# Performance work log

Hardware: AMD Instinct MI355X
Metric: run time of the kernel (lower is better)

## Reference

```python
import jax, jax.numpy as jnp
import numpy as np

B, N, C = 16, 1024, 768
H, HD = 9, 64  # num_active_heads, head_dim


def setup_inputs() -> dict:
    key = jax.random.key(0)
    ks = jax.random.split(key, 5)
    x = jax.random.normal(ks[0], (B, N, C), dtype=jnp.float32)
    qkv_w = jax.random.normal(ks[1], (3 * H * HD, C), dtype=jnp.float32) * (1.0 / np.sqrt(C))
    qkv_b = jax.random.normal(ks[2], (3 * H * HD,), dtype=jnp.float32) * 0.02
    proj_w = jax.random.normal(ks[3], (C, H * HD), dtype=jnp.float32) * (1.0 / np.sqrt(H * HD))
    proj_b = jax.random.normal(ks[4], (C,), dtype=jnp.float32) * 0.02
    return {"x": x, "qkv_w": qkv_w, "qkv_b": qkv_b, "proj_w": proj_w, "proj_b": proj_b}


def reference(x, qkv_w, qkv_b, proj_w, proj_b):
    b, n, c = x.shape
    # qkv projection: [B,N,3*H*HD] -> [3,B,H,N,HD]
    qkv = (x @ qkv_w.T + qkv_b).reshape(b, n, 3, H, HD).transpose(2, 0, 3, 1, 4)
    q, k, v = qkv[0], qkv[1], qkv[2]
    scale = HD ** -0.5
    attn = jnp.einsum('bhqd,bhkd->bhqk', q, k) * scale  # [B,H,N,N]
    attn = jax.nn.softmax(attn, axis=-1)
    out = jnp.einsum('bhqk,bhkd->bhqd', attn, v)  # [B,H,N,HD]
    out = out.transpose(0, 2, 1, 3).reshape(b, n, H * HD)
    return out @ proj_w.T + proj_b
```

## Files before the change

### kernel.cpp

```cpp
#include <hip/hip_runtime.h>


typedef _Float16 f16x8 __attribute__((ext_vector_type(8)));
typedef _Float16 f16x4 __attribute__((ext_vector_type(4)));
typedef __fp16   h16x2 __attribute__((ext_vector_type(2)));
typedef float    f32x4 __attribute__((ext_vector_type(4)));

#define MFMA16(a, b, c) __builtin_amdgcn_mfma_f32_16x16x32_f16(a, b, c, 0, 0, 0)

__device__ __forceinline__ void gld16(const _Float16* g, _Float16* l) {
  __builtin_amdgcn_global_load_lds((const __attribute__((address_space(1))) void*)g,
                                   (__attribute__((address_space(3))) void*)l, 16, 0, 0);
}

__global__ __launch_bounds__(256) void cvt_swz(const float* __restrict__ src,
                                               _Float16* __restrict__ dst,
                                               int rows_src, int cpr, int total) {
  const int g = blockIdx.x * 256 + threadIdx.x;
  if (g >= total) return;
  const int row = g / cpr;
  const int c = g - row * cpr;
  const int L = cpr * 8;
  const int pos = (c & ~7) | ((c ^ row) & 7);
  union { f16x8 v; h16x2 h[4]; } u;
  if (row < rows_src) {
    const float4 a = *(const float4*)(src + row * L + c * 8);
    const float4 b = *(const float4*)(src + row * L + c * 8 + 4);
    u.h[0] = __builtin_amdgcn_cvt_pkrtz(a.x, a.y);
    u.h[1] = __builtin_amdgcn_cvt_pkrtz(a.z, a.w);
    u.h[2] = __builtin_amdgcn_cvt_pkrtz(b.x, b.y);
    u.h[3] = __builtin_amdgcn_cvt_pkrtz(b.z, b.w);
  } else {
    u.v = (f16x8){};
  }
  *(f16x8*)(dst + row * L + pos * 8) = u.v;
}

__global__ __launch_bounds__(256, 4) void gemm1_qkv(const _Float16* __restrict__ A,
                                                    const _Float16* __restrict__ Bw,
                                                    const float* __restrict__ bias,
                                                    _Float16* __restrict__ Qo,
                                                    _Float16* __restrict__ Ko,
                                                    _Float16* __restrict__ Vt) {
  __shared__ __align__(16) _Float16 As[128 * 64];
  __shared__ __align__(16) _Float16 Bs[128 * 64];
  const int tid = threadIdx.x;
  const int wave = tid >> 6, lane = tid & 63;
  const int lo = lane & 15, hi = lane >> 4;
  const int wm = (wave >> 1) * 64, wn = (wave & 1) * 64;
  const int m0 = blockIdx.x * 128, n0 = blockIdx.y * 128;
  f32x4 acc[4][4] = {};
  for (int k0 = 0; k0 < 768; k0 += 64) {
    __syncthreads();
    #pragma unroll
    for (int j = 0; j < 4; ++j) {
      const int seg = wave * 4 + j;
      const int gr = seg * 8 + (lane >> 3), gc = (lane & 7) << 3;
      gld16(A + (m0 + gr) * 768 + k0 + gc, As + seg * 512);
      gld16(Bw + (n0 + gr) * 768 + k0 + gc, Bs + seg * 512);
    }
    __syncthreads();
    #pragma unroll
    for (int ks = 0; ks < 2; ++ks) {
      f16x8 af[4], bf[4];
      const int p = ((ks * 4 + hi) ^ (lo & 7)) << 3;
      #pragma unroll
      for (int t = 0; t < 4; ++t) {
        af[t] = *(const f16x8*)(As + (wm + t * 16 + lo) * 64 + p);
        bf[t] = *(const f16x8*)(Bs + (wn + t * 16 + lo) * 64 + p);
      }
      #pragma unroll
      for (int mt = 0; mt < 4; ++mt)
        #pragma unroll
        for (int nt = 0; nt < 4; ++nt)
          acc[mt][nt] = MFMA16(af[mt], bf[nt], acc[mt][nt]);
    }
  }
  const int b = m0 >> 10;
  const int nrbase = (m0 & 1023) + wm;
  #pragma unroll
  for (int nt = 0; nt < 4; ++nt) {
    const int n = n0 + wn + nt * 16 + lo;
    if (n < 1728) {
      const float bv = bias[n];
      const int t3 = n / 576;
      const int rem = n - t3 * 576;
      const int hh = rem >> 6, d = rem & 63;
      const int bh16 = (b * 9 + hh) << 16;
      if (t3 == 2) {
        _Float16* dv = Vt + bh16 + d * 1024;
        #pragma unroll
        for (int mt = 0; mt < 4; ++mt) {
          const int nr = nrbase + mt * 16 + hi * 4;
          const int c = nr >> 3;
          const int pos = (c & ~7) | ((c ^ d) & 7);
          union { f16x4 v; h16x2 h[2]; } u;
          u.h[0] = __builtin_amdgcn_cvt_pkrtz(acc[mt][nt][0] + bv, acc[mt][nt][1] + bv);
          u.h[1] = __builtin_amdgcn_cvt_pkrtz(acc[mt][nt][2] + bv, acc[mt][nt][3] + bv);
          *(f16x4*)(dv + pos * 8 + (nr & 7)) = u.v;
        }
      } else if (t3 == 1) {
        _Float16* dk = Ko + bh16;
        const int ch = d >> 3, dl = d & 7;
        #pragma unroll
        for (int mt = 0; mt < 4; ++mt) {
          const int nr = nrbase + mt * 16 + hi * 4;
          #pragma unroll
          for (int i = 0; i < 4; ++i) {
            const int t = nr + i;
            dk[t * 64 + ((ch ^ (t & 7)) << 3) + dl] = (_Float16)(acc[mt][nt][i] + bv);
          }
        }
      } else {
        _Float16* dq = Qo + bh16 + d;
        #pragma unroll
        for (int mt = 0; mt < 4; ++mt) {
          const int nr = nrbase + mt * 16 + hi * 4;
          #pragma unroll
          for (int i = 0; i < 4; ++i)
            dq[(nr + i) * 64] = (_Float16)(acc[mt][nt][i] + bv);
        }
      }
    }
  }
}

__global__ __launch_bounds__(256, 4) void attn_fused(const _Float16* __restrict__ Qg,
                                                     const _Float16* __restrict__ Kg,
                                                     const _Float16* __restrict__ Vtg,
                                                     _Float16* __restrict__ Og) {
  __shared__ __align__(16) _Float16 Ks[128 * 64];
  __shared__ __align__(16) _Float16 Vts[64 * 128];
  const int tid = threadIdx.x;
  const int wave = tid >> 6, lane = tid & 63;
  const int lo = lane & 15, hi = lane >> 4;
  const int bh = blockIdx.x;
  const int q0 = blockIdx.y * 64;
  const _Float16* Qp  = Qg + (bh << 16);
  const _Float16* Kp  = Kg + (bh << 16);
  const _Float16* Vtp = Vtg + (bh << 16);

  #pragma unroll
  for (int it = 0; it < 2; ++it) {
    const int c = it * 256 + tid;
    const int row = c >> 3, ch = c & 7;
    *(uint4*)(Ks + row * 64 + ((ch ^ (row & 7)) << 3)) =
        *(const uint4*)(Qp + (q0 + row) * 64 + ch * 8);
  }
  __syncthreads();
  f16x8 qf[2];
  #pragma unroll
  for (int ks = 0; ks < 2; ++ks)
    qf[ks] = *(const f16x8*)(Ks + (wave * 16 + lo) * 64 + (((ks * 4 + hi) ^ (lo & 7)) << 3));

  _Float16* Ps = Ks + wave * 2048;
  float m_run = -1e30f, l_run = 0.f;
  f32x4 accO[4] = {};
  const float cs = 0.125f * 1.44269504f;

  for (int t0 = 0; t0 < 1024; t0 += 128) {
    __syncthreads();
    #pragma unroll
    for (int j = 0; j < 4; ++j) {
      const int seg = wave * 4 + j;
      gld16(Kp + (t0 + seg * 8 + (lane >> 3)) * 64 + ((lane & 7) << 3), Ks + seg * 512);
      gld16(Vtp + (seg * 4 + (lane >> 4)) * 1024 + t0 + ((lane & 15) << 3), Vts + seg * 512);
    }
    __syncthreads();

    f32x4 sacc[8] = {};
    #pragma unroll
    for (int tt = 0; tt < 8; ++tt)
      #pragma unroll
      for (int ks = 0; ks < 2; ++ks) {
        const f16x8 kf = *(const f16x8*)(Ks + (tt * 16 + lo) * 64 + (((ks * 4 + hi) ^ (lo & 7)) << 3));
        sacc[tt] = MFMA16(kf, qf[ks], sacc[tt]);
      }
    __syncthreads();

    float rmax = -1e30f;
    #pragma unroll
    for (int tt = 0; tt < 8; ++tt)
      rmax = fmaxf(rmax, fmaxf(fmaxf(sacc[tt][0], sacc[tt][1]), fmaxf(sacc[tt][2], sacc[tt][3])));
    rmax = fmaxf(rmax, __shfl_xor(rmax, 16, 64));
    rmax = fmaxf(rmax, __shfl_xor(rmax, 32, 64));
    const float mnew = fmaxf(m_run, rmax * cs);
    const float alpha = __builtin_amdgcn_exp2f(m_run - mnew);
    float rsum = 0.f;
    #pragma unroll
    for (int tt = 0; tt < 8; ++tt) {
      const float p0 = __builtin_amdgcn_exp2f(fmaf(sacc[tt][0], cs, -mnew));
      const float p1 = __builtin_amdgcn_exp2f(fmaf(sacc[tt][1], cs, -mnew));
      const float p2 = __builtin_amdgcn_exp2f(fmaf(sacc[tt][2], cs, -mnew));
      const float p3 = __builtin_amdgcn_exp2f(fmaf(sacc[tt][3], cs, -mnew));
      rsum += (p0 + p1) + (p2 + p3);
      union { f16x4 v; h16x2 h[2]; } u;
      u.h[0] = __builtin_amdgcn_cvt_pkrtz(p0, p1);
      u.h[1] = __builtin_amdgcn_cvt_pkrtz(p2, p3);
      const int c = 2 * tt + (hi >> 1);
      *(f16x4*)(Ps + lo * 128 + (((c & 8) | ((c ^ lo) & 7)) << 3) + ((hi & 1) << 2)) = u.v;
    }
    rsum += __shfl_xor(rsum, 16, 64);
    rsum += __shfl_xor(rsum, 32, 64);
    l_run = l_run * alpha + rsum;
    m_run = mnew;
    #pragma unroll
    for (int dt = 0; dt < 4; ++dt) accO[dt] *= alpha;

    #pragma unroll
    for (int ks2 = 0; ks2 < 4; ++ks2) {
      const int c = 4 * ks2 + hi;
      const f16x8 pf = *(const f16x8*)(Ps + lo * 128 + (((c & 8) | ((c ^ lo) & 7)) << 3));
      #pragma unroll
      for (int dt = 0; dt < 4; ++dt) {
        const int dd = dt * 16 + lo;
        const f16x8 vf = *(const f16x8*)(Vts + dd * 128 + (((c & 8) | ((c ^ dd) & 7)) << 3));
        accO[dt] = MFMA16(vf, pf, accO[dt]);
      }
    }
  }
  const float inv = 1.f / l_run;
  const int b = bh / 9, hh = bh - b * 9;
  const int rq = (b << 10) + q0 + wave * 16 + lo;
  #pragma unroll
  for (int dt = 0; dt < 4; ++dt) {
    union { f16x4 v; h16x2 h[2]; } u;
    u.h[0] = __builtin_amdgcn_cvt_pkrtz(accO[dt][0] * inv, accO[dt][1] * inv);
    u.h[1] = __builtin_amdgcn_cvt_pkrtz(accO[dt][2] * inv, accO[dt][3] * inv);
    const int c = hh * 8 + dt * 2 + (hi >> 1);
    const int pos = (c & ~7) | ((c ^ rq) & 7);
    *(f16x4*)(Og + rq * 576 + pos * 8 + ((hi & 1) << 2)) = u.v;
  }
}

__global__ __launch_bounds__(256, 4) void gemm3_proj(const _Float16* __restrict__ A,
                                                     const _Float16* __restrict__ Bw,
                                                     const float* __restrict__ bias,
                                                     float* __restrict__ out) {
  __shared__ __align__(16) _Float16 As[128 * 64];
  __shared__ __align__(16) _Float16 Bs[128 * 64];
  const int tid = threadIdx.x;
  const int wave = tid >> 6, lane = tid & 63;
  const int lo = lane & 15, hi = lane >> 4;
  const int wm = (wave >> 1) * 64, wn = (wave & 1) * 64;
  const int m0 = blockIdx.x * 128, n0 = blockIdx.y * 128;
  f32x4 acc[4][4] = {};
  for (int k0 = 0; k0 < 576; k0 += 64) {
    __syncthreads();
    #pragma unroll
    for (int j = 0; j < 4; ++j) {
      const int seg = wave * 4 + j;
      const int gr = seg * 8 + (lane >> 3), gc = (lane & 7) << 3;
      gld16(A + (m0 + gr) * 576 + k0 + gc, As + seg * 512);
      gld16(Bw + (n0 + gr) * 576 + k0 + gc, Bs + seg * 512);
    }
    __syncthreads();
    #pragma unroll
    for (int ks = 0; ks < 2; ++ks) {
      f16x8 af[4], bf[4];
      const int p = ((ks * 4 + hi) ^ (lo & 7)) << 3;
      #pragma unroll
      for (int t = 0; t < 4; ++t) {
        af[t] = *(const f16x8*)(As + (wm + t * 16 + lo) * 64 + p);
        bf[t] = *(const f16x8*)(Bs + (wn + t * 16 + lo) * 64 + p);
      }
      #pragma unroll
      for (int mt = 0; mt < 4; ++mt)
        #pragma unroll
        for (int nt = 0; nt < 4; ++nt)
          acc[mt][nt] = MFMA16(af[mt], bf[nt], acc[mt][nt]);
    }
  }
  #pragma unroll
  for (int nt = 0; nt < 4; ++nt) {
    const int n = n0 + wn + nt * 16 + lo;
    const float bv = bias[n];
    #pragma unroll
    for (int mt = 0; mt < 4; ++mt) {
      const int mrow = m0 + wm + mt * 16 + hi * 4;
      #pragma unroll
      for (int i = 0; i < 4; ++i)
        out[(mrow + i) * 768 + n] = acc[mt][nt][i] + bv;
    }
  }
}

extern "C" void kernel_launch(void* const* d_in, const int* in_sizes, int n_in,
                              void* d_out, int out_size, void* d_ws, size_t ws_size,
                              hipStream_t stream) {
  const float* x      = (const float*)d_in[0];
  const float* qkv_w  = (const float*)d_in[1];
  const float* qkv_b  = (const float*)d_in[2];
  const float* proj_w = (const float*)d_in[3];
  const float* proj_b = (const float*)d_in[4];
  float* out = (float*)d_out;

  char* ws = (char*)d_ws;
  _Float16* x16 = (_Float16*)(ws + 0);
  _Float16* w1p = (_Float16*)(ws + 25165824);
  _Float16* w2h = (_Float16*)(ws + 27918336);
  _Float16* Qh  = (_Float16*)(ws + 28803072);
  _Float16* Kh  = (_Float16*)(ws + 47677440);
  _Float16* Vth = (_Float16*)(ws + 66551808);
  _Float16* Oh  = (_Float16*)(ws + 85426176);

  cvt_swz<<<6144, 256, 0, stream>>>(x, x16, 16384, 96, 16384 * 96);
  cvt_swz<<<672, 256, 0, stream>>>(qkv_w, w1p, 1728, 96, 1792 * 96);
  cvt_swz<<<216, 256, 0, stream>>>(proj_w, w2h, 768, 72, 768 * 72);
  gemm1_qkv<<<dim3(128, 14), 256, 0, stream>>>(x16, w1p, qkv_b, Qh, Kh, Vth);
  attn_fused<<<dim3(144, 16), 256, 0, stream>>>(Qh, Kh, Vth, Oh);
  gemm3_proj<<<dim3(128, 6), 256, 0, stream>>>(Oh, w2h, proj_b, out);
}
```

Measured before the change: 260.2 us.

## Double-buffer K/V tiles in attention with async prefetch and XCD-aware block mapping

```diff
diff --git a/kernel.cpp b/kernel.cpp
--- a/kernel.cpp
+++ b/kernel.cpp
@@ -129,58 +129,55 @@
                                                      const _Float16* __restrict__ Kg,
                                                      const _Float16* __restrict__ Vtg,
                                                      _Float16* __restrict__ Og) {
-  __shared__ __align__(16) _Float16 Ks[128 * 64];
-  __shared__ __align__(16) _Float16 Vts[64 * 128];
+  __shared__ __align__(16) _Float16 Ks[2][64 * 64];
+  __shared__ __align__(16) _Float16 Vts[2][64 * 64];
+  __shared__ __align__(16) _Float16 Ps[4][16 * 64];
   const int tid = threadIdx.x;
   const int wave = tid >> 6, lane = tid & 63;
   const int lo = lane & 15, hi = lane >> 4;
-  const int bh = blockIdx.x;
-  const int q0 = blockIdx.y * 64;
+  const int bid = blockIdx.x;
+  const int xcd = bid & 7, idx = bid >> 3;
+  const int bh = xcd * 18 + (idx >> 4);
+  const int q0 = (idx & 15) << 6;
   const _Float16* Qp  = Qg + (bh << 16);
   const _Float16* Kp  = Kg + (bh << 16);
   const _Float16* Vtp = Vtg + (bh << 16);
 
-  #pragma unroll
-  for (int it = 0; it < 2; ++it) {
-    const int c = it * 256 + tid;
-    const int row = c >> 3, ch = c & 7;
-    *(uint4*)(Ks + row * 64 + ((ch ^ (row & 7)) << 3)) =
-        *(const uint4*)(Qp + (q0 + row) * 64 + ch * 8);
-  }
-  __syncthreads();
+  auto issue = [&](int t0, int nb) {
+    #pragma unroll
+    for (int j = 0; j < 2; ++j) {
+      const int seg = wave * 2 + j;
+      gld16(Kp + (t0 + seg * 8 + (lane >> 3)) * 64 + ((lane & 7) << 3), &Ks[nb][seg * 512]);
+      gld16(Vtp + (seg * 8 + (lane >> 3)) * 1024 + t0 + ((lane & 7) << 3), &Vts[nb][seg * 512]);
+    }
+  };
+
+  issue(0, 0);
+
   f16x8 qf[2];
-  #pragma unroll
-  for (int ks = 0; ks < 2; ++ks)
-    qf[ks] = *(const f16x8*)(Ks + (wave * 16 + lo) * 64 + (((ks * 4 + hi) ^ (lo & 7)) << 3));
-
-  _Float16* Ps = Ks + wave * 2048;
+  const _Float16* qrow = Qp + (q0 + wave * 16 + lo) * 64;
+  qf[0] = *(const f16x8*)(qrow + hi * 8);
+  qf[1] = *(const f16x8*)(qrow + (4 + hi) * 8);
+
   float m_run = -1e30f, l_run = 0.f;
   f32x4 accO[4] = {};
   const float cs = 0.125f * 1.44269504f;
-
-  for (int t0 = 0; t0 < 1024; t0 += 128) {
-    __syncthreads();
-    #pragma unroll
-    for (int j = 0; j < 4; ++j) {
-      const int seg = wave * 4 + j;
-      gld16(Kp + (t0 + seg * 8 + (lane >> 3)) * 64 + ((lane & 7) << 3), Ks + seg * 512);
-      gld16(Vtp + (seg * 4 + (lane >> 4)) * 1024 + t0 + ((lane & 15) << 3), Vts + seg * 512);
-    }
-    __syncthreads();
-
-    f32x4 sacc[8] = {};
-    #pragma unroll
-    for (int tt = 0; tt < 8; ++tt)
+  _Float16* Pw = Ps[wave];
+
+  auto compute = [&](int cb) {
+    const _Float16* Kc = Ks[cb];
+    const _Float16* Vc = Vts[cb];
+    f32x4 sacc[4] = {};
+    #pragma unroll
+    for (int tt = 0; tt < 4; ++tt)
       #pragma unroll
       for (int ks = 0; ks < 2; ++ks) {
-        const f16x8 kf = *(const f16x8*)(Ks + (tt * 16 + lo) * 64 + (((ks * 4 + hi) ^ (lo & 7)) << 3));
+        const f16x8 kf = *(const f16x8*)(Kc + (tt * 16 + lo) * 64 + (((ks * 4 + hi) ^ (lo & 7)) << 3));
         sacc[tt] = MFMA16(kf, qf[ks], sacc[tt]);
       }
-    __syncthreads();
-
     float rmax = -1e30f;
     #pragma unroll
-    for (int tt = 0; tt < 8; ++tt)
+    for (int tt = 0; tt < 4; ++tt)
       rmax = fmaxf(rmax, fmaxf(fmaxf(sacc[tt][0], sacc[tt][1]), fmaxf(sacc[tt][2], sacc[tt][3])));
     rmax = fmaxf(rmax, __shfl_xor(rmax, 16, 64));
     rmax = fmaxf(rmax, __shfl_xor(rmax, 32, 64));
@@ -188,7 +185,7 @@
     const float alpha = __builtin_amdgcn_exp2f(m_run - mnew);
     float rsum = 0.f;
     #pragma unroll
-    for (int tt = 0; tt < 8; ++tt) {
+    for (int tt = 0; tt < 4; ++tt) {
       const float p0 = __builtin_amdgcn_exp2f(fmaf(sacc[tt][0], cs, -mnew));
       const float p1 = __builtin_amdgcn_exp2f(fmaf(sacc[tt][1], cs, -mnew));
       const float p2 = __builtin_amdgcn_exp2f(fmaf(sacc[tt][2], cs, -mnew));
@@ -198,7 +195,7 @@
       u.h[0] = __builtin_amdgcn_cvt_pkrtz(p0, p1);
       u.h[1] = __builtin_amdgcn_cvt_pkrtz(p2, p3);
       const int c = 2 * tt + (hi >> 1);
-      *(f16x4*)(Ps + lo * 128 + (((c & 8) | ((c ^ lo) & 7)) << 3) + ((hi & 1) << 2)) = u.v;
+      *(f16x4*)(Pw + lo * 64 + (((c ^ lo) & 7) << 3) + ((hi & 1) << 2)) = u.v;
     }
     rsum += __shfl_xor(rsum, 16, 64);
     rsum += __shfl_xor(rsum, 32, 64);
@@ -208,17 +205,40 @@
     for (int dt = 0; dt < 4; ++dt) accO[dt] *= alpha;
 
     #pragma unroll
-    for (int ks2 = 0; ks2 < 4; ++ks2) {
+    for (int ks2 = 0; ks2 < 2; ++ks2) {
       const int c = 4 * ks2 + hi;
-      const f16x8 pf = *(const f16x8*)(Ps + lo * 128 + (((c & 8) | ((c ^ lo) & 7)) << 3));
+      const f16x8 pf = *(const f16x8*)(Pw + lo * 64 + (((c ^ lo) & 7) << 3));
       #pragma unroll
       for (int dt = 0; dt < 4; ++dt) {
         const int dd = dt * 16 + lo;
-        const f16x8 vf = *(const f16x8*)(Vts + dd * 128 + (((c & 8) | ((c ^ dd) & 7)) << 3));
+        const f16x8 vf = *(const f16x8*)(Vc + dd * 64 + (((c ^ dd) & 7) << 3));
         accO[dt] = MFMA16(vf, pf, accO[dt]);
       }
     }
-  }
+  };
+
+  auto step = [&](int tnext0, int cb, bool pre) {
+    if (pre) {
+      issue(tnext0, cb ^ 1);
+      asm volatile("s_waitcnt vmcnt(4)" ::: "memory");
+    } else {
+      asm volatile("s_waitcnt vmcnt(0)" ::: "memory");
+    }
+    __builtin_amdgcn_sched_barrier(0);
+    __builtin_amdgcn_s_barrier();
+    compute(cb);
+    __builtin_amdgcn_sched_barrier(0);
+    __builtin_amdgcn_s_barrier();
+  };
+
+  #pragma unroll 1
+  for (int it = 0; it < 7; ++it) {
+    step((2 * it + 1) << 6, 0, true);
+    step((2 * it + 2) << 6, 1, true);
+  }
+  step(15 << 6, 0, true);
+  step(0, 1, false);
+
   const float inv = 1.f / l_run;
   const int b = bh / 9, hh = bh - b * 9;
   const int rq = (b << 10) + q0 + wave * 16 + lo;
@@ -308,6 +328,6 @@
   cvt_swz<<<672, 256, 0, stream>>>(qkv_w, w1p, 1728, 96, 1792 * 96);
   cvt_swz<<<216, 256, 0, stream>>>(proj_w, w2h, 768, 72, 768 * 72);
   gemm1_qkv<<<dim3(128, 14), 256, 0, stream>>>(x16, w1p, qkv_b, Qh, Kh, Vth);
-  attn_fused<<<dim3(144, 16), 256, 0, stream>>>(Qh, Kh, Vth, Oh);
+  attn_fused<<<2304, 256, 0, stream>>>(Qh, Kh, Vth, Oh);
   gemm3_proj<<<dim3(128, 6), 256, 0, stream>>>(Oh, w2h, proj_b, out);
 }
```

Measured after the change: 256.2 us. About the same (-1.5%).
